# Performance work log

Measured on AMD Instinct MI355X. Metric: run time of the kernel, lower is better.

Reference implementation:

```python
import jax, jax.numpy as jnp
import numpy as np
import math


def setup_inputs() -> dict:
    key = jax.random.key(0)
    kq, kk, kv = jax.random.split(key, 3)
    B, N, H = 4, 4096, 128
    return {
        "q": jax.random.normal(kq, (B, N, H), dtype=jnp.float32),
        "k": jax.random.normal(kk, (B, N, H), dtype=jnp.float32),
        "v": jax.random.normal(kv, (B, N, H), dtype=jnp.float32),
        "block_size": 128,
    }


def reference(q, k, v, block_size):
    # The torch module is an exact online-softmax (flash-attention) tiling of
    # full, unmasked softmax attention: out = softmax(q k^T / sqrt(H)) @ v.
    # The block-wise m/l running updates compute the identical result, so the
    # clean dense form below is the faithful math.
    H = q.shape[-1]
    scale = 1.0 / math.sqrt(H)
    s = jnp.einsum("bnh,bmh->bnm", q, k) * scale  # [B, N, N]
    p = jax.nn.softmax(s, axis=-1)                 # numerically stable softmax
    return jnp.einsum("bnm,bmh->bnh", p, v)
```

## Files before the change

kernel.cpp:

```cpp
#include <hip/hip_runtime.h>

typedef __attribute__((ext_vector_type(4))) float f32x4;
typedef __attribute__((ext_vector_type(8))) short short8;

#define DEVI static __device__ __forceinline__

constexpr int B_ = 4;
constexpr int N_ = 4096;
constexpr int H_ = 128;
constexpr size_t ELEMS = (size_t)B_ * N_ * H_;
constexpr size_t TSB = ELEMS * 2;

constexpr int QT = 128;
constexpr int KVB = 64;
constexpr int NTH = 256;

DEVI unsigned short f2bf(float x) {
  union { float f; unsigned u; } a; a.f = x;
  unsigned u = a.u;
  return (unsigned short)((u + 0x7FFFu + ((u >> 16) & 1u)) >> 16);
}

DEVI int swz(int byteoff, int row) { return byteoff ^ ((row & 7) << 4); }

DEVI void gl_lds16(const void* g, void* l) {
  __builtin_amdgcn_global_load_lds(
      (const __attribute__((address_space(1))) void*)g,
      (__attribute__((address_space(3))) void*)l, 16, 0, 0);
}

__global__ void conv_qk(const float* __restrict__ q, const float* __restrict__ k,
                        unsigned short* __restrict__ qb, unsigned short* __restrict__ kb) {
  const float qscale = 0.08838834764831845f * 1.4426950408889634f;
  size_t i = (size_t)blockIdx.x * blockDim.x + threadIdx.x;
  {
    const float4* s = (const float4*)q + 2 * i;
    float4 a = s[0], b = s[1];
    short8 t;
    t[0] = (short)f2bf(a.x * qscale); t[1] = (short)f2bf(a.y * qscale);
    t[2] = (short)f2bf(a.z * qscale); t[3] = (short)f2bf(a.w * qscale);
    t[4] = (short)f2bf(b.x * qscale); t[5] = (short)f2bf(b.y * qscale);
    t[6] = (short)f2bf(b.z * qscale); t[7] = (short)f2bf(b.w * qscale);
    *(short8*)(qb + i * 8) = t;
  }
  {
    const float4* s = (const float4*)k + 2 * i;
    float4 a = s[0], b = s[1];
    short8 t;
    t[0] = (short)f2bf(a.x); t[1] = (short)f2bf(a.y);
    t[2] = (short)f2bf(a.z); t[3] = (short)f2bf(a.w);
    t[4] = (short)f2bf(b.x); t[5] = (short)f2bf(b.y);
    t[6] = (short)f2bf(b.z); t[7] = (short)f2bf(b.w);
    *(short8*)(kb + i * 8) = t;
  }
}

__global__ void conv_vt(const float* __restrict__ v, unsigned short* __restrict__ vt) {
  __shared__ unsigned short T[64][72];
  const int n0 = blockIdx.x * 64, h0 = blockIdx.y * 64, b = blockIdx.z;
  const int t = threadIdx.x;
  const int c4 = t & 15, r = t >> 4;
#pragma unroll
  for (int i = 0; i < 4; ++i) {
    int n = n0 + r + 16 * i;
    float4 val = *(const float4*)(v + ((size_t)b * N_ + n) * H_ + h0 + 4 * c4);
    T[4 * c4 + 0][r + 16 * i] = f2bf(val.x);
    T[4 * c4 + 1][r + 16 * i] = f2bf(val.y);
    T[4 * c4 + 2][r + 16 * i] = f2bf(val.z);
    T[4 * c4 + 3][r + 16 * i] = f2bf(val.w);
  }
  __syncthreads();
  const int c8 = t & 7, hr = t >> 3;
#pragma unroll
  for (int i = 0; i < 2; ++i) {
    int hl = hr + 32 * i;
    short8 val = *(const short8*)(&T[hl][8 * c8]);
    *(short8*)(vt + ((size_t)b * H_ + h0 + hl) * N_ + n0 + 8 * c8) = val;
  }
}

template <int KS>
__global__ __launch_bounds__(NTH, 2)
void fattn_v5(const unsigned short* __restrict__ qws,
              const unsigned short* __restrict__ kws,
              const unsigned short* __restrict__ vtws,
              float* __restrict__ opart, float* __restrict__ mlpart) {
  constexpr int KVRANGE = N_ / KS;
  constexpr int NST = KVRANGE / KVB;

  __shared__ __align__(16) char smem[73728];
  char* Kb0 = smem;
  char* Vb0 = smem + 32768;

  const int tid = threadIdx.x, wave = tid >> 6, lane = tid & 63;
  const int l15 = lane & 15, l4 = lane >> 4;

  const int bid = blockIdx.x;
  int x, b, z;
  if (KS == 4) {
    int pair = (bid & 7) * 2 + ((bid >> 3) & 1);
    x = bid >> 4;
    b = pair >> 2;
    z = pair & 3;
  } else {
    int pair = bid & 7;
    x = bid >> 3;
    b = pair >> 1;
    z = pair & 1;
  }

  const int qg0 = x * QT + wave * 32;
  const size_t kvz = (size_t)z * KVRANGE;
  const int swzm = (l15 & 7) << 4;
  char* Pw = smem + 65536 + wave * 2048;

  const unsigned short* qp0 = qws + ((size_t)b * N_ + qg0 + l15) * H_;
  short8 qf0[4], qf1[4];
#pragma unroll
  for (int kc = 0; kc < 4; ++kc) {
    qf0[kc] = *(const short8*)(qp0 + 8 * l4 + 32 * kc);
    qf1[kc] = *(const short8*)(qp0 + 16 * H_ + 8 * l4 + 32 * kc);
  }

  f32x4 O0[8], O1[8];
#pragma unroll
  for (int i = 0; i < 8; ++i) { O0[i] = (f32x4){0,0,0,0}; O1[i] = (f32x4){0,0,0,0}; }
  float m0 = 0.f, l0 = 0.f, m1 = 0.f, l1 = 0.f;

  const char* kbase = (const char*)(kws + ((size_t)b * N_ + kvz) * H_);
  const char* vbase = (const char*)(vtws + (size_t)b * H_ * N_) + kvz * 2;

  auto stage = [&](int buf, int step) {
    const char* kt = kbase + (size_t)step * KVB * H_ * 2;
    char* kd = Kb0 + buf * 16384;
#pragma unroll
    for (int i = 0; i < 4; ++i) {
      int off = (tid + 256 * i) * 16;
      int row = off >> 8, col = off & 255;
      gl_lds16(kt + row * 256 + (col ^ ((row & 7) << 4)), kd + off);
    }
    const char* vt0 = vbase + (size_t)step * KVB * 2;
    char* vd = Vb0 + buf * 16384;
#pragma unroll
    for (int i = 0; i < 4; ++i) {
      int off = (tid + 256 * i) * 16;
      int h = off >> 7, colb = off & 127;
      gl_lds16(vt0 + (size_t)h * (N_ * 2) + (colb ^ ((h & 7) << 4)), vd + off);
    }
  };

  auto softmax_prep = [&](f32x4 (&S)[4], float& m, float& l, f32x4 (&O)[8], short8 (&pf)[2]) {
    float p[16];
#pragma unroll
    for (int ct = 0; ct < 4; ++ct)
#pragma unroll
      for (int r = 0; r < 4; ++r)
        p[4 * ct + r] = __builtin_amdgcn_exp2f(S[ct][r] - m);
    float a0 = fmaxf(p[0], p[1]), a1 = fmaxf(p[2], p[3]);
    float a2 = fmaxf(p[4], p[5]), a3 = fmaxf(p[6], p[7]);
    float a4 = fmaxf(p[8], p[9]), a5 = fmaxf(p[10], p[11]);
    float a6 = fmaxf(p[12], p[13]), a7 = fmaxf(p[14], p[15]);
    float b0 = fmaxf(a0, a1), b1 = fmaxf(a2, a3), b2 = fmaxf(a4, a5), b3 = fmaxf(a6, a7);
    float mx = fmaxf(fmaxf(b0, b1), fmaxf(b2, b3));
    mx = fmaxf(mx, __shfl_xor(mx, 16));
    mx = fmaxf(mx, __shfl_xor(mx, 32));
    float s0 = (p[0] + p[1]) + (p[2] + p[3]);
    float s1 = (p[4] + p[5]) + (p[6] + p[7]);
    float s2 = (p[8] + p[9]) + (p[10] + p[11]);
    float s3 = (p[12] + p[13]) + (p[14] + p[15]);
    float rs = (s0 + s1) + (s2 + s3);
    rs += __shfl_xor(rs, 16);
    rs += __shfl_xor(rs, 32);
    if (__builtin_expect(!__all(mx <= 256.f), 0)) {
      float sc = fmaxf(mx, 1.f);
      float ai = 1.f / sc;
      m += __builtin_amdgcn_logf(sc);
      l = (l + rs) * ai;
#pragma unroll
      for (int i = 0; i < 16; ++i) p[i] *= ai;
#pragma unroll
      for (int i = 0; i < 8; ++i) O[i] = O[i] * ai;
    } else {
      l += rs;
    }
#pragma unroll
    for (int ct = 0; ct < 4; ++ct) {
      uint2 pk;
      pk.x = (unsigned)f2bf(p[4 * ct]) | ((unsigned)f2bf(p[4 * ct + 1]) << 16);
      pk.y = (unsigned)f2bf(p[4 * ct + 2]) | ((unsigned)f2bf(p[4 * ct + 3]) << 16);
      *(uint2*)(Pw + ((l15 * 128 + 32 * ct + 8 * l4) ^ swzm)) = pk;
    }
    pf[0] = *(const short8*)(Pw + ((l15 * 128 + 16 * l4) ^ swzm));
    pf[1] = *(const short8*)(Pw + ((l15 * 128 + 16 * l4 + 64) ^ swzm));
  };

  stage(0, 0);
  __syncthreads();
  int cur = 0;

  for (int st = 0; st < NST; ++st) {
    if (st + 1 < NST) stage(cur ^ 1, st + 1);

    const char* Kl = Kb0 + cur * 16384;
    const char* Vl = Vb0 + cur * 16384;

    f32x4 S0[4], S1[4];
#pragma unroll
    for (int ct = 0; ct < 4; ++ct) { S0[ct] = (f32x4){0,0,0,0}; S1[ct] = (f32x4){0,0,0,0}; }
    __builtin_amdgcn_s_setprio(1);
#pragma unroll
    for (int kc = 0; kc < 4; ++kc) {
#pragma unroll
      for (int ct = 0; ct < 4; ++ct) {
        int kr = 16 * ct + l15;
        short8 af = *(const short8*)(Kl + ((kr * 256 + 16 * l4 + 64 * kc) ^ ((kr & 7) << 4)));
        S0[ct] = __builtin_amdgcn_mfma_f32_16x16x32_bf16(af, qf0[kc], S0[ct], 0, 0, 0);
        S1[ct] = __builtin_amdgcn_mfma_f32_16x16x32_bf16(af, qf1[kc], S1[ct], 0, 0, 0);
      }
    }
    __builtin_amdgcn_s_setprio(0);

    short8 pf0[2], pf1[2];
    softmax_prep(S0, m0, l0, O0, pf0);
    softmax_prep(S1, m1, l1, O1, pf1);

    __builtin_amdgcn_s_setprio(1);
#pragma unroll
    for (int kc2 = 0; kc2 < 2; ++kc2) {
#pragma unroll
      for (int ct2 = 0; ct2 < 8; ++ct2) {
        int hr = 16 * ct2 + l15;
        short8 vf = *(const short8*)(Vl + ((hr * 128 + 16 * l4 + 64 * kc2) ^ ((hr & 7) << 4)));
        O0[ct2] = __builtin_amdgcn_mfma_f32_16x16x32_bf16(vf, pf0[kc2], O0[ct2], 0, 0, 0);
        O1[ct2] = __builtin_amdgcn_mfma_f32_16x16x32_bf16(vf, pf1[kc2], O1[ct2], 0, 0, 0);
      }
    }
    __builtin_amdgcn_s_setprio(0);

    __syncthreads();
    cur ^= 1;
  }

#pragma unroll
  for (int ct2 = 0; ct2 < 8; ++ct2) {
    int q0 = wave * 32 + l15;
    *(f32x4*)(smem + q0 * 512 + ((64 * ct2 + 16 * l4) ^ ((q0 & 7) << 4))) = O0[ct2];
    int q1 = q0 + 16;
    *(f32x4*)(smem + q1 * 512 + ((64 * ct2 + 16 * l4) ^ ((q1 & 7) << 4))) = O1[ct2];
  }
  if (l4 == 0) {
    size_t r0 = ((size_t)z * B_ + b) * N_ + qg0 + l15;
    mlpart[2 * r0] = m0;
    mlpart[2 * r0 + 1] = l0;
    mlpart[2 * (r0 + 16)] = m1;
    mlpart[2 * (r0 + 16) + 1] = l1;
  }
  __syncthreads();
  float* od = opart + (((size_t)z * B_ + b) * N_ + (size_t)x * QT) * H_;
#pragma unroll
  for (int i = 0; i < 16; ++i) {
    int off = (tid + 256 * i) * 16;
    int q = off >> 9, colb = off & 511;
    f32x4 val = *(const f32x4*)(smem + q * 512 + (colb ^ ((q & 7) << 4)));
    *(f32x4*)((char*)od + (size_t)q * 512 + colb) = val;
  }
}

template <int KS>
__global__ void combine_k(const float* __restrict__ opart, const float* __restrict__ mlpart,
                          float* __restrict__ out) {
  const int t = threadIdx.x;
  size_t row = (size_t)blockIdx.x * 8 + (t >> 5);
  int hc = (t & 31) * 4;
  float mz[KS], lz[KS];
  float mi = -__builtin_inff();
#pragma unroll
  for (int z = 0; z < KS; ++z) {
    size_t r = (size_t)z * B_ * N_ + row;
    mz[z] = mlpart[2 * r];
    lz[z] = mlpart[2 * r + 1];
    mi = fmaxf(mi, mz[z]);
  }
  float lsum = 0.f;
  float az[KS];
#pragma unroll
  for (int z = 0; z < KS; ++z) {
    az[z] = __builtin_amdgcn_exp2f(mz[z] - mi);
    lsum += az[z] * lz[z];
  }
  float rinv = 1.f / lsum;
  f32x4 acc = (f32x4){0, 0, 0, 0};
#pragma unroll
  for (int z = 0; z < KS; ++z) {
    f32x4 oz = *(const f32x4*)(opart + (size_t)z * B_ * N_ * H_ + row * H_ + hc);
    acc = acc + oz * (az[z] * rinv);
  }
  *(f32x4*)(out + row * H_ + hc) = acc;
}

constexpr int FB_QTILE = 64;
constexpr int FB_KVSTEP = 128;
constexpr int FB_KVHALF = 64;
constexpr int FB_NTH = 512;
constexpr int FB_NSTEPS = N_ / FB_KVSTEP;

__global__ __launch_bounds__(FB_NTH, 2)
void fattn_fast(const unsigned short* __restrict__ qws,
                const unsigned short* __restrict__ kws,
                const unsigned short* __restrict__ vtws,
                float* __restrict__ out) {
  __shared__ unsigned short Kbuf[2][FB_KVSTEP * H_];
  __shared__ unsigned short Vbuf[2][H_ * FB_KVSTEP];
  __shared__ unsigned short Plds[8][16 * FB_KVHALF];
  __shared__ float MLlds[4][16][2];

  const int tid = threadIdx.x;
  const int wave = tid >> 6;
  const int lane = tid & 63;
  const int l15 = lane & 15;
  const int l4 = lane >> 4;
  const int sub = wave & 3;
  const int grp = wave >> 2;

  const int b = blockIdx.y;
  const int qbase = blockIdx.x * FB_QTILE;

  const unsigned short* qp = qws + ((size_t)b * N_ + qbase + sub * 16 + l15) * H_;
  short8 qfrag[4];
#pragma unroll
  for (int kc = 0; kc < 4; ++kc)
    qfrag[kc] = *(const short8*)(qp + 8 * l4 + 32 * kc);

  f32x4 Oacc[8];
#pragma unroll
  for (int i = 0; i < 8; ++i) Oacc[i] = (f32x4){0.f, 0.f, 0.f, 0.f};
  float mrun[4], lrun[4];
#pragma unroll
  for (int r = 0; r < 4; ++r) { mrun[r] = -__builtin_inff(); lrun[r] = 0.f; }

  const char* kbase = (const char*)(kws + (size_t)b * N_ * H_);
  const char* vbase = (const char*)(vtws + (size_t)b * H_ * N_);
  const int kvbase = grp * FB_KVHALF;
  char* pbase = (char*)Plds[wave];

  auto stage = [&](int buf, int step) {
    const char* ktile = kbase + (size_t)step * FB_KVSTEP * H_ * 2;
#pragma unroll
    for (int i = 0; i < 4; ++i) {
      int chunk = wave * 4 + i;
      int off = chunk * 1024 + lane * 16;
      int row = off >> 8, col = off & 255;
      gl_lds16(ktile + row * 256 + (col ^ ((row & 7) << 4)),
               (char*)Kbuf[buf] + chunk * 1024);
    }
#pragma unroll
    for (int i = 0; i < 4; ++i) {
      int chunk = wave * 4 + i;
      int h = chunk * 4 + (lane >> 4);
      int colb = (lane & 15) * 16;
      gl_lds16(vbase + (size_t)h * (N_ * 2) + (size_t)step * 256 + (colb ^ ((h & 7) << 4)),
               (char*)Vbuf[buf] + chunk * 1024);
    }
  };

  int cur = 0;
  stage(0, 0);
  __syncthreads();

  for (int step = 0; step < FB_NSTEPS; ++step) {
    if (step + 1 < FB_NSTEPS) stage(cur ^ 1, step + 1);

    const char* Kl = (const char*)Kbuf[cur];
    const char* Vl = (const char*)Vbuf[cur];

    f32x4 S[4];
#pragma unroll
    for (int ct = 0; ct < 4; ++ct) S[ct] = (f32x4){0.f, 0.f, 0.f, 0.f};
#pragma unroll
    for (int ct = 0; ct < 4; ++ct) {
      int kvrow = kvbase + ct * 16 + l15;
#pragma unroll
      for (int kc = 0; kc < 4; ++kc) {
        short8 bfrag = *(const short8*)(Kl +
            swz(kvrow * 256 + (8 * l4 + 32 * kc) * 2, kvrow));
        S[ct] = __builtin_amdgcn_mfma_f32_16x16x32_bf16(qfrag[kc], bfrag, S[ct], 0, 0, 0);
      }
    }

    float mnew[4];
#pragma unroll
    for (int r = 0; r < 4; ++r) {
      float mx = fmaxf(fmaxf(S[0][r], S[1][r]), fmaxf(S[2][r], S[3][r]));
      mx = fmaxf(mx, __shfl_xor(mx, 1));
      mx = fmaxf(mx, __shfl_xor(mx, 2));
      mx = fmaxf(mx, __shfl_xor(mx, 4));
      mx = fmaxf(mx, __shfl_xor(mx, 8));
      mnew[r] = mx;
    }
    float alpha[4];
#pragma unroll
    for (int r = 0; r < 4; ++r) {
      float mi = fmaxf(mrun[r], mnew[r]);
      alpha[r] = __builtin_amdgcn_exp2f(mrun[r] - mi);
      mrun[r] = mi;
    }
    float rsum[4] = {0.f, 0.f, 0.f, 0.f};
    unsigned short pb[4][4];
#pragma unroll
    for (int ct = 0; ct < 4; ++ct)
#pragma unroll
      for (int r = 0; r < 4; ++r) {
        float pv = __builtin_amdgcn_exp2f(S[ct][r] - mrun[r]);
        rsum[r] += pv;
        pb[ct][r] = f2bf(pv);
      }
#pragma unroll
    for (int r = 0; r < 4; ++r) {
      float s = rsum[r];
      s += __shfl_xor(s, 1); s += __shfl_xor(s, 2);
      s += __shfl_xor(s, 4); s += __shfl_xor(s, 8);
      lrun[r] = lrun[r] * alpha[r] + s;
    }
#pragma unroll
    for (int ct2 = 0; ct2 < 8; ++ct2)
#pragma unroll
      for (int r = 0; r < 4; ++r) Oacc[ct2][r] *= alpha[r];

#pragma unroll
    for (int ct = 0; ct < 4; ++ct)
#pragma unroll
      for (int r = 0; r < 4; ++r) {
        int qrow = 4 * l4 + r;
        int kv = l15 + 16 * ct;
        *(unsigned short*)(pbase + swz(qrow * 128 + kv * 2, qrow)) = pb[ct][r];
      }

#pragma unroll
    for (int kc2 = 0; kc2 < 2; ++kc2) {
      short8 afrag = *(const short8*)(pbase +
          swz(l15 * 128 + (8 * l4 + 32 * kc2) * 2, l15));
#pragma unroll
      for (int ct2 = 0; ct2 < 8; ++ct2) {
        int h = l15 + 16 * ct2;
        short8 bfrag = *(const short8*)(Vl +
            swz(h * 256 + (kvbase + 8 * l4 + 32 * kc2) * 2, h));
        Oacc[ct2] = __builtin_amdgcn_mfma_f32_16x16x32_bf16(afrag, bfrag, Oacc[ct2], 0, 0, 0);
      }
    }

    __syncthreads();
    cur ^= 1;
  }

  __syncthreads();
  float* mergeO = (float*)Kbuf;
  if (grp == 1) {
#pragma unroll
    for (int ct2 = 0; ct2 < 8; ++ct2)
#pragma unroll
      for (int r = 0; r < 4; ++r) {
        int qrow = 4 * l4 + r, h = l15 + 16 * ct2;
        mergeO[(sub * 16 + qrow) * H_ + h] = Oacc[ct2][r];
      }
    if (l15 == 0) {
#pragma unroll
      for (int r = 0; r < 4; ++r) {
        int qrow = 4 * l4 + r;
        MLlds[sub][qrow][0] = mrun[r];
        MLlds[sub][qrow][1] = lrun[r];
      }
    }
  }
  __syncthreads();
  if (grp == 0) {
    float aA[4], aB[4], rl[4];
#pragma unroll
    for (int r = 0; r < 4; ++r) {
      int qrow = 4 * l4 + r;
      float mB = MLlds[sub][qrow][0], lB = MLlds[sub][qrow][1];
      float mi = fmaxf(mrun[r], mB);
      aA[r] = __builtin_amdgcn_exp2f(mrun[r] - mi);
      aB[r] = __builtin_amdgcn_exp2f(mB - mi);
      rl[r] = 1.f / (lrun[r] * aA[r] + lB * aB[r]);
    }
    float* outp = out + ((size_t)b * N_ + qbase + sub * 16) * H_;
#pragma unroll
    for (int ct2 = 0; ct2 < 8; ++ct2)
#pragma unroll
      for (int r = 0; r < 4; ++r) {
        int qrow = 4 * l4 + r, h = l15 + 16 * ct2;
        float ob = mergeO[(sub * 16 + qrow) * H_ + h];
        outp[(size_t)qrow * H_ + h] = (Oacc[ct2][r] * aA[r] + ob * aB[r]) * rl[r];
      }
  }
}

extern "C" void kernel_launch(void* const* d_in, const int* in_sizes, int n_in,
                              void* d_out, int out_size, void* d_ws, size_t ws_size,
                              hipStream_t stream) {
  const float* q = (const float*)d_in[0];
  const float* k = (const float*)d_in[1];
  const float* v = (const float*)d_in[2];
  float* out = (float*)d_out;

  auto need = [](int ks) {
    return 3 * TSB + (size_t)ks * ELEMS * 4 + (size_t)ks * B_ * N_ * 2 * 4;
  };

  if (ws_size >= need(4)) {
    unsigned short* qb = (unsigned short*)d_ws;
    unsigned short* kb = qb + ELEMS;
    unsigned short* vt = kb + ELEMS;
    float* opart = (float*)((char*)d_ws + 3 * TSB);
    float* mlpart = opart + (size_t)4 * ELEMS;
    conv_qk<<<dim3((unsigned)(ELEMS / 8 / 256)), dim3(256), 0, stream>>>(q, k, qb, kb);
    conv_vt<<<dim3(N_ / 64, H_ / 64, B_), dim3(256), 0, stream>>>(v, vt);
    fattn_v5<4><<<dim3(512), dim3(NTH), 0, stream>>>(qb, kb, vt, opart, mlpart);
    combine_k<4><<<dim3(B_ * N_ / 8), dim3(256), 0, stream>>>(opart, mlpart, out);
  } else if (ws_size >= need(2)) {
    unsigned short* qb = (unsigned short*)d_ws;
    unsigned short* kb = qb + ELEMS;
    unsigned short* vt = kb + ELEMS;
    float* opart = (float*)((char*)d_ws + 3 * TSB);
    float* mlpart = opart + (size_t)2 * ELEMS;
    conv_qk<<<dim3((unsigned)(ELEMS / 8 / 256)), dim3(256), 0, stream>>>(q, k, qb, kb);
    conv_vt<<<dim3(N_ / 64, H_ / 64, B_), dim3(256), 0, stream>>>(v, vt);
    fattn_v5<2><<<dim3(256), dim3(NTH), 0, stream>>>(qb, kb, vt, opart, mlpart);
    combine_k<2><<<dim3(B_ * N_ / 8), dim3(256), 0, stream>>>(opart, mlpart, out);
  } else if (ws_size >= 3 * TSB) {
    unsigned short* qb = (unsigned short*)d_ws;
    unsigned short* kb = qb + ELEMS;
    unsigned short* vt = kb + ELEMS;
    conv_qk<<<dim3((unsigned)(ELEMS / 8 / 256)), dim3(256), 0, stream>>>(q, k, qb, kb);
    conv_vt<<<dim3(N_ / 64, H_ / 64, B_), dim3(256), 0, stream>>>(v, vt);
    fattn_fast<<<dim3(N_ / FB_QTILE, B_), dim3(FB_NTH), 0, stream>>>(qb, kb, vt, out);
  }
}
```

Before: 72.00 us.

## Halve KV tile to raise occupancy, interleave PV per half, direct output stores

Shrinks the KV block from 64 to 32 rows, cutting LDS per workgroup so four blocks can fit per CU (launch bounds raised from 2 to 4). The two query halves now each run softmax followed immediately by their PV MFMAs, so matrix work overlaps with the other half's softmax. It also uses the hardware packed bf16 convert instruction and writes O partials straight from registers instead of staging them through LDS. In exchange it doubles the number of barriers and loop iterations, and the tighter launch bound pressures registers and may cause spills.

```diff
diff --git a/kernel.cpp b/kernel.cpp
--- a/kernel.cpp
+++ b/kernel.cpp
@@ -12,13 +12,19 @@
 constexpr size_t TSB = ELEMS * 2;
 
 constexpr int QT = 128;
-constexpr int KVB = 64;
+constexpr int KVB = 32;
 constexpr int NTH = 256;
 
 DEVI unsigned short f2bf(float x) {
   union { float f; unsigned u; } a; a.f = x;
   unsigned u = a.u;
   return (unsigned short)((u + 0x7FFFu + ((u >> 16) & 1u)) >> 16);
+}
+
+DEVI unsigned cvt_pk_bf16(float lo, float hi) {
+  unsigned w;
+  asm("v_cvt_pk_bf16_f32 %0, %1, %2" : "=v"(w) : "v"(lo), "v"(hi));
+  return w;
 }
 
 DEVI int swz(int byteoff, int row) { return byteoff ^ ((row & 7) << 4); }
@@ -80,17 +86,17 @@
 }
 
 template <int KS>
-__global__ __launch_bounds__(NTH, 2)
-void fattn_v5(const unsigned short* __restrict__ qws,
+__global__ __launch_bounds__(NTH, 4)
+void fattn_v6(const unsigned short* __restrict__ qws,
               const unsigned short* __restrict__ kws,
               const unsigned short* __restrict__ vtws,
               float* __restrict__ opart, float* __restrict__ mlpart) {
   constexpr int KVRANGE = N_ / KS;
   constexpr int NST = KVRANGE / KVB;
 
-  __shared__ __align__(16) char smem[73728];
+  __shared__ __align__(16) char smem[36864];
   char* Kb0 = smem;
-  char* Vb0 = smem + 32768;
+  char* Vb0 = smem + 16384;
 
   const int tid = threadIdx.x, wave = tid >> 6, lane = tid & 63;
   const int l15 = lane & 15, l4 = lane >> 4;
@@ -111,8 +117,8 @@
 
   const int qg0 = x * QT + wave * 32;
   const size_t kvz = (size_t)z * KVRANGE;
-  const int swzm = (l15 & 7) << 4;
-  char* Pw = smem + 65536 + wave * 2048;
+  char* Pw = smem + 32768 + wave * 1024;
+  const int pswz = (l15 & 3) << 4;
 
   const unsigned short* qp0 = qws + ((size_t)b * N_ + qg0 + l15) * H_;
   short8 qf0[4], qf1[4];
@@ -132,43 +138,36 @@
 
   auto stage = [&](int buf, int step) {
     const char* kt = kbase + (size_t)step * KVB * H_ * 2;
-    char* kd = Kb0 + buf * 16384;
-#pragma unroll
-    for (int i = 0; i < 4; ++i) {
+    char* kd = Kb0 + buf * 8192;
+#pragma unroll
+    for (int i = 0; i < 2; ++i) {
       int off = (tid + 256 * i) * 16;
       int row = off >> 8, col = off & 255;
       gl_lds16(kt + row * 256 + (col ^ ((row & 7) << 4)), kd + off);
     }
     const char* vt0 = vbase + (size_t)step * KVB * 2;
-    char* vd = Vb0 + buf * 16384;
-#pragma unroll
-    for (int i = 0; i < 4; ++i) {
+    char* vd = Vb0 + buf * 8192;
+#pragma unroll
+    for (int i = 0; i < 2; ++i) {
       int off = (tid + 256 * i) * 16;
-      int h = off >> 7, colb = off & 127;
-      gl_lds16(vt0 + (size_t)h * (N_ * 2) + (colb ^ ((h & 7) << 4)), vd + off);
+      int h = off >> 6, colb = off & 63;
+      gl_lds16(vt0 + (size_t)h * (N_ * 2) + (colb ^ ((h & 3) << 4)), vd + off);
     }
   };
 
-  auto softmax_prep = [&](f32x4 (&S)[4], float& m, float& l, f32x4 (&O)[8], short8 (&pf)[2]) {
-    float p[16];
-#pragma unroll
-    for (int ct = 0; ct < 4; ++ct)
+  auto softmax_prep = [&](f32x4 (&S)[2], float& m, float& l, f32x4 (&O)[8], short8& pf) {
+    float p[8];
+#pragma unroll
+    for (int ct = 0; ct < 2; ++ct)
 #pragma unroll
       for (int r = 0; r < 4; ++r)
         p[4 * ct + r] = __builtin_amdgcn_exp2f(S[ct][r] - m);
     float a0 = fmaxf(p[0], p[1]), a1 = fmaxf(p[2], p[3]);
     float a2 = fmaxf(p[4], p[5]), a3 = fmaxf(p[6], p[7]);
-    float a4 = fmaxf(p[8], p[9]), a5 = fmaxf(p[10], p[11]);
-    float a6 = fmaxf(p[12], p[13]), a7 = fmaxf(p[14], p[15]);
-    float b0 = fmaxf(a0, a1), b1 = fmaxf(a2, a3), b2 = fmaxf(a4, a5), b3 = fmaxf(a6, a7);
-    float mx = fmaxf(fmaxf(b0, b1), fmaxf(b2, b3));
+    float mx = fmaxf(fmaxf(a0, a1), fmaxf(a2, a3));
     mx = fmaxf(mx, __shfl_xor(mx, 16));
     mx = fmaxf(mx, __shfl_xor(mx, 32));
-    float s0 = (p[0] + p[1]) + (p[2] + p[3]);
-    float s1 = (p[4] + p[5]) + (p[6] + p[7]);
-    float s2 = (p[8] + p[9]) + (p[10] + p[11]);
-    float s3 = (p[12] + p[13]) + (p[14] + p[15]);
-    float rs = (s0 + s1) + (s2 + s3);
+    float rs = ((p[0] + p[1]) + (p[2] + p[3])) + ((p[4] + p[5]) + (p[6] + p[7]));
     rs += __shfl_xor(rs, 16);
     rs += __shfl_xor(rs, 32);
     if (__builtin_expect(!__all(mx <= 256.f), 0)) {
@@ -177,21 +176,20 @@
       m += __builtin_amdgcn_logf(sc);
       l = (l + rs) * ai;
 #pragma unroll
-      for (int i = 0; i < 16; ++i) p[i] *= ai;
+      for (int i = 0; i < 8; ++i) p[i] *= ai;
 #pragma unroll
       for (int i = 0; i < 8; ++i) O[i] = O[i] * ai;
     } else {
       l += rs;
     }
 #pragma unroll
-    for (int ct = 0; ct < 4; ++ct) {
+    for (int ct = 0; ct < 2; ++ct) {
       uint2 pk;
-      pk.x = (unsigned)f2bf(p[4 * ct]) | ((unsigned)f2bf(p[4 * ct + 1]) << 16);
-      pk.y = (unsigned)f2bf(p[4 * ct + 2]) | ((unsigned)f2bf(p[4 * ct + 3]) << 16);
-      *(uint2*)(Pw + ((l15 * 128 + 32 * ct + 8 * l4) ^ swzm)) = pk;
-    }
-    pf[0] = *(const short8*)(Pw + ((l15 * 128 + 16 * l4) ^ swzm));
-    pf[1] = *(const short8*)(Pw + ((l15 * 128 + 16 * l4 + 64) ^ swzm));
+      pk.x = cvt_pk_bf16(p[4 * ct], p[4 * ct + 1]);
+      pk.y = cvt_pk_bf16(p[4 * ct + 2], p[4 * ct + 3]);
+      *(uint2*)(Pw + ((l15 * 64 + 32 * ct + 8 * l4) ^ pswz)) = pk;
+    }
+    pf = *(const short8*)(Pw + ((l15 * 64 + 16 * l4) ^ pswz));
   };
 
   stage(0, 0);
@@ -201,17 +199,17 @@
   for (int st = 0; st < NST; ++st) {
     if (st + 1 < NST) stage(cur ^ 1, st + 1);
 
-    const char* Kl = Kb0 + cur * 16384;
-    const char* Vl = Vb0 + cur * 16384;
-
-    f32x4 S0[4], S1[4];
-#pragma unroll
-    for (int ct = 0; ct < 4; ++ct) { S0[ct] = (f32x4){0,0,0,0}; S1[ct] = (f32x4){0,0,0,0}; }
+    const char* Kl = Kb0 + cur * 8192;
+    const char* Vl = Vb0 + cur * 8192;
+
+    f32x4 S0[2], S1[2];
+#pragma unroll
+    for (int ct = 0; ct < 2; ++ct) { S0[ct] = (f32x4){0,0,0,0}; S1[ct] = (f32x4){0,0,0,0}; }
     __builtin_amdgcn_s_setprio(1);
 #pragma unroll
     for (int kc = 0; kc < 4; ++kc) {
 #pragma unroll
-      for (int ct = 0; ct < 4; ++ct) {
+      for (int ct = 0; ct < 2; ++ct) {
         int kr = 16 * ct + l15;
         short8 af = *(const short8*)(Kl + ((kr * 256 + 16 * l4 + 64 * kc) ^ ((kr & 7) << 4)));
         S0[ct] = __builtin_amdgcn_mfma_f32_16x16x32_bf16(af, qf0[kc], S0[ct], 0, 0, 0);
@@ -220,34 +218,26 @@
     }
     __builtin_amdgcn_s_setprio(0);
 
-    short8 pf0[2], pf1[2];
+    short8 pf0, pf1;
     softmax_prep(S0, m0, l0, O0, pf0);
+#pragma unroll
+    for (int ct2 = 0; ct2 < 8; ++ct2) {
+      int hr = 16 * ct2 + l15;
+      short8 vf = *(const short8*)(Vl + ((hr * 64 + 16 * l4) ^ ((hr & 3) << 4)));
+      O0[ct2] = __builtin_amdgcn_mfma_f32_16x16x32_bf16(vf, pf0, O0[ct2], 0, 0, 0);
+    }
     softmax_prep(S1, m1, l1, O1, pf1);
-
-    __builtin_amdgcn_s_setprio(1);
-#pragma unroll
-    for (int kc2 = 0; kc2 < 2; ++kc2) {
-#pragma unroll
-      for (int ct2 = 0; ct2 < 8; ++ct2) {
-        int hr = 16 * ct2 + l15;
-        short8 vf = *(const short8*)(Vl + ((hr * 128 + 16 * l4 + 64 * kc2) ^ ((hr & 7) << 4)));
-        O0[ct2] = __builtin_amdgcn_mfma_f32_16x16x32_bf16(vf, pf0[kc2], O0[ct2], 0, 0, 0);
-        O1[ct2] = __builtin_amdgcn_mfma_f32_16x16x32_bf16(vf, pf1[kc2], O1[ct2], 0, 0, 0);
-      }
-    }
-    __builtin_amdgcn_s_setprio(0);
+#pragma unroll
+    for (int ct2 = 0; ct2 < 8; ++ct2) {
+      int hr = 16 * ct2 + l15;
+      short8 vf = *(const short8*)(Vl + ((hr * 64 + 16 * l4) ^ ((hr & 3) << 4)));
+      O1[ct2] = __builtin_amdgcn_mfma_f32_16x16x32_bf16(vf, pf1, O1[ct2], 0, 0, 0);
+    }
 
     __syncthreads();
     cur ^= 1;
   }
 
-#pragma unroll
-  for (int ct2 = 0; ct2 < 8; ++ct2) {
-    int q0 = wave * 32 + l15;
-    *(f32x4*)(smem + q0 * 512 + ((64 * ct2 + 16 * l4) ^ ((q0 & 7) << 4))) = O0[ct2];
-    int q1 = q0 + 16;
-    *(f32x4*)(smem + q1 * 512 + ((64 * ct2 + 16 * l4) ^ ((q1 & 7) << 4))) = O1[ct2];
-  }
   if (l4 == 0) {
     size_t r0 = ((size_t)z * B_ + b) * N_ + qg0 + l15;
     mlpart[2 * r0] = m0;
@@ -255,14 +245,12 @@
     mlpart[2 * (r0 + 16)] = m1;
     mlpart[2 * (r0 + 16) + 1] = l1;
   }
-  __syncthreads();
-  float* od = opart + (((size_t)z * B_ + b) * N_ + (size_t)x * QT) * H_;
-#pragma unroll
-  for (int i = 0; i < 16; ++i) {
-    int off = (tid + 256 * i) * 16;
-    int q = off >> 9, colb = off & 511;
-    f32x4 val = *(const f32x4*)(smem + q * 512 + (colb ^ ((q & 7) << 4)));
-    *(f32x4*)((char*)od + (size_t)q * 512 + colb) = val;
+  float* od0 = opart + (((size_t)z * B_ + b) * N_ + qg0 + l15) * H_ + 4 * l4;
+  float* od1 = od0 + 16 * H_;
+#pragma unroll
+  for (int ct2 = 0; ct2 < 8; ++ct2) {
+    *(f32x4*)(od0 + 16 * ct2) = O0[ct2];
+    *(f32x4*)(od1 + 16 * ct2) = O1[ct2];
   }
 }
 
@@ -382,7 +370,7 @@
 #pragma unroll
       for (int kc = 0; kc < 4; ++kc) {
         short8 bfrag = *(const short8*)(Kl +
-            swz(kvrow * 256 + (8 * l4 + 32 * kc) * 2, kvrow));
+            ((kvrow * 256 + (8 * l4 + 32 * kc) * 2) ^ ((kvrow & 7) << 4)));
         S[ct] = __builtin_amdgcn_mfma_f32_16x16x32_bf16(qfrag[kc], bfrag, S[ct], 0, 0, 0);
       }
     }
@@ -432,18 +420,18 @@
       for (int r = 0; r < 4; ++r) {
         int qrow = 4 * l4 + r;
         int kv = l15 + 16 * ct;
-        *(unsigned short*)(pbase + swz(qrow * 128 + kv * 2, qrow)) = pb[ct][r];
+        *(unsigned short*)(pbase + ((qrow * 128 + kv * 2) ^ ((qrow & 7) << 4))) = pb[ct][r];
       }
 
 #pragma unroll
     for (int kc2 = 0; kc2 < 2; ++kc2) {
       short8 afrag = *(const short8*)(pbase +
-          swz(l15 * 128 + (8 * l4 + 32 * kc2) * 2, l15));
+          ((l15 * 128 + (8 * l4 + 32 * kc2) * 2) ^ ((l15 & 7) << 4)));
 #pragma unroll
       for (int ct2 = 0; ct2 < 8; ++ct2) {
         int h = l15 + 16 * ct2;
         short8 bfrag = *(const short8*)(Vl +
-            swz(h * 256 + (kvbase + 8 * l4 + 32 * kc2) * 2, h));
+            ((h * 256 + (kvbase + 8 * l4 + 32 * kc2) * 2) ^ ((h & 7) << 4)));
         Oacc[ct2] = __builtin_amdgcn_mfma_f32_16x16x32_bf16(afrag, bfrag, Oacc[ct2], 0, 0, 0);
       }
     }
@@ -515,7 +503,7 @@
     float* mlpart = opart + (size_t)4 * ELEMS;
     conv_qk<<<dim3((unsigned)(ELEMS / 8 / 256)), dim3(256), 0, stream>>>(q, k, qb, kb);
     conv_vt<<<dim3(N_ / 64, H_ / 64, B_), dim3(256), 0, stream>>>(v, vt);
-    fattn_v5<4><<<dim3(512), dim3(NTH), 0, stream>>>(qb, kb, vt, opart, mlpart);
+    fattn_v6<4><<<dim3(512), dim3(NTH), 0, stream>>>(qb, kb, vt, opart, mlpart);
     combine_k<4><<<dim3(B_ * N_ / 8), dim3(256), 0, stream>>>(opart, mlpart, out);
   } else if (ws_size >= need(2)) {
     unsigned short* qb = (unsigned short*)d_ws;
@@ -525,7 +513,7 @@
     float* mlpart = opart + (size_t)2 * ELEMS;
     conv_qk<<<dim3((unsigned)(ELEMS / 8 / 256)), dim3(256), 0, stream>>>(q, k, qb, kb);
     conv_vt<<<dim3(N_ / 64, H_ / 64, B_), dim3(256), 0, stream>>>(v, vt);
-    fattn_v5<2><<<dim3(256), dim3(NTH), 0, stream>>>(qb, kb, vt, opart, mlpart);
+    fattn_v6<2><<<dim3(256), dim3(NTH), 0, stream>>>(qb, kb, vt, opart, mlpart);
     combine_k<2><<<dim3(B_ * N_ / 8), dim3(256), 0, stream>>>(opart, mlpart, out);
   } else if (ws_size >= 3 * TSB) {
     unsigned short* qb = (unsigned short*)d_ws;
```

After: 246.6 us. 243% more time.
